# Optimization experiments

Hardware: AMD Instinct MI355X
Metric: run time of the kernel (lower is better)

## Reference

```python
import jax, jax.numpy as jnp
import numpy as np

BN_EPS = 1e-3          # nn.BatchNorm1d(..., eps=0.001)
NUM_PILLARS = 600000   # M = total occupied pillars across the batch
N_POINTS = 3_000_000
C_IN, C_OUT = 10, 64


def setup_inputs() -> dict:
    key = jax.random.key(0)
    k1, k2, k3 = jax.random.split(key, 3)
    pts_feature = jax.random.normal(k1, (N_POINTS, C_IN), dtype=jnp.float32)
    point_pillar_indices = jax.random.randint(k2, (N_POINTS,), 0, NUM_PILLARS, dtype=jnp.int32)
    # Linear(C_IN, C_OUT, bias=False), kaiming_normal init
    W = jax.random.normal(k3, (C_IN, C_OUT), dtype=jnp.float32) * np.sqrt(2.0 / C_IN)
    # BatchNorm1d in eval mode (running stats)
    gamma = jnp.ones((C_OUT,), jnp.float32)
    beta = jnp.zeros((C_OUT,), jnp.float32)
    run_mean = jnp.zeros((C_OUT,), jnp.float32)
    run_var = jnp.ones((C_OUT,), jnp.float32)
    return {"pts_feature": pts_feature, "point_pillar_indices": point_pillar_indices,
            "W": W, "gamma": gamma, "beta": beta, "run_mean": run_mean, "run_var": run_var}


def reference(pts_feature, point_pillar_indices, W, gamma, beta, run_mean, run_var):
    # shared MLP: Linear(no bias) -> BatchNorm1d(eval) -> ReLU, fused per-point
    h = pts_feature @ W                                        # (N, C_OUT)
    h = gamma * (h - run_mean) * jax.lax.rsqrt(run_var + BN_EPS) + beta
    h = jax.nn.relu(h)
    # scatter_max over irregular pillar ids -> (M, C_OUT)
    pooled = jax.ops.segment_max(h, point_pillar_indices, num_segments=NUM_PILLARS)
    # torch scatter_max leaves empty pillars at 0; jax gives -inf -> replace
    return jnp.where(jnp.isfinite(pooled), pooled, 0.0)
```

## Files before the change

kernel.cpp:

```cpp
#include <hip/hip_runtime.h>

#define C_IN 10
#define C_OUT 64
#define BN_EPS 1e-3f

#define BP    128
#define CB    256
#define NBMAX 4704
#define WIN   256
#define FSTR  12
#define MAXB  1536
#define TS    2048


__global__ __launch_bounds__(256) void k1_hist(const int* __restrict__ idx, int n, int chunk,
                                               unsigned* __restrict__ ghist, int NB) {
    __shared__ unsigned h[NBMAX];
    const int b = blockIdx.x, t = threadIdx.x;
    for (int i = t; i < NB; i += 256) h[i] = 0u;
    __syncthreads();
    const int lo = b * chunk;
    const int hi = min(n, lo + chunk);
    for (int i = lo + t; i < hi; i += 256)
        atomicAdd(&h[((unsigned)idx[i]) >> 7], 1u);
    __syncthreads();
    for (int k = t; k < NB; k += 256) ghist[(size_t)k * CB + b] = h[k];
}

__global__ __launch_bounds__(256) void k2a_reduce(const unsigned* __restrict__ g, int G,
                                                  unsigned* __restrict__ tsum) {
    __shared__ unsigned s[256];
    const int t = threadIdx.x;
    const int base = blockIdx.x * TS + t * 8;
    unsigned acc = 0;
#pragma unroll
    for (int j = 0; j < 8; ++j) { int gi = base + j; if (gi < G) acc += g[gi]; }
    s[t] = acc; __syncthreads();
    for (int off = 128; off > 0; off >>= 1) { if (t < off) s[t] += s[t + off]; __syncthreads(); }
    if (t == 0) tsum[blockIdx.x] = s[0];
}

__global__ __launch_bounds__(256) void k2b_scan(unsigned* __restrict__ tsum, int nt) {
    __shared__ unsigned partial[256], basev[256];
    const int t = threadIdx.x;
    const int per = (nt + 255) / 256;
    const int lo = t * per, hi = min(nt, lo + per);
    unsigned s = 0;
    for (int i = lo; i < hi; ++i) s += tsum[i];
    partial[t] = s; __syncthreads();
    if (t == 0) { unsigned a = 0; for (int k = 0; k < 256; ++k) { basev[k] = a; a += partial[k]; } }
    __syncthreads();
    unsigned a = basev[t];
    for (int i = lo; i < hi; ++i) { unsigned v = tsum[i]; tsum[i] = a; a += v; }
}

__global__ __launch_bounds__(256) void k2c_apply(unsigned* __restrict__ g, int G,
                                                 const unsigned* __restrict__ tsum,
                                                 unsigned* __restrict__ bstart, int NB, int n) {
    __shared__ unsigned s[256];
    const int t = threadIdx.x;
    const int base = blockIdx.x * TS + t * 8;
    unsigned v[8]; unsigned acc = 0;
#pragma unroll
    for (int j = 0; j < 8; ++j) { int gi = base + j; v[j] = (gi < G) ? g[gi] : 0u; acc += v[j]; }
    s[t] = acc; __syncthreads();
    for (int off = 1; off < 256; off <<= 1) {
        unsigned x = (t >= off) ? s[t - off] : 0u; __syncthreads();
        s[t] += x; __syncthreads();
    }
    unsigned excl = ((t == 0) ? 0u : s[t - 1]) + tsum[blockIdx.x];
#pragma unroll
    for (int j = 0; j < 8; ++j) {
        int gi = base + j;
        if (gi < G) {
            g[gi] = excl;
            if ((gi & (CB - 1)) == 0) bstart[gi / CB] = excl;
            excl += v[j];
        }
    }
    if (blockIdx.x == 0 && t == 0) bstart[NB] = (unsigned)n;
}

__global__ __launch_bounds__(256) void k3_scatter(const int* __restrict__ idx, int n, int chunk,
                                                  const unsigned* __restrict__ scanned,
                                                  unsigned* __restrict__ rec, int NB) {
    __shared__ unsigned cnt[NBMAX];
    __shared__ unsigned basel[NBMAX];
    const int b = blockIdx.x, t = threadIdx.x;
    for (int k = t; k < NB; k += 256) { basel[k] = scanned[(size_t)k * CB + b]; cnt[k] = 0u; }
    __syncthreads();
    const int lo = b * chunk, hi = min(n, lo + chunk);
    for (int i = lo + t; i < hi; i += 256) {
        unsigned pid = (unsigned)idx[i];
        unsigned k = pid >> 7;
        unsigned r = atomicAdd(&cnt[k], 1u);
        rec[basel[k] + r] = ((pid & 127u) << 22) | (unsigned)i;
    }
}

__global__ __launch_bounds__(256) void pool_sorted_kernel(
    const float* __restrict__ pts,
    const unsigned* __restrict__ rec,
    const unsigned* __restrict__ bstart,
    const float* __restrict__ W,
    const float* __restrict__ gamma, const float* __restrict__ beta,
    const float* __restrict__ mean, const float* __restrict__ var,
    float* __restrict__ out, int M)
{
    __shared__ float4  feat4[WIN * FSTR / 4];
    __shared__ unsigned seg_end[BP];
    __shared__ unsigned cnt[BP];
    __shared__ unsigned short ord[MAXB];
    __shared__ unsigned char  lpa[MAXB];
    float* feat = (float*)feat4;

    const int b = blockIdx.x;
    const int t = threadIdx.x;
    const int lane = t & 63;
    const int w = t >> 6;

    const unsigned base = bstart[b];
    const int T  = (int)(bstart[b + 1] - base);
    const int Tc = T < MAXB ? T : MAXB;
    const int npl = min(BP, M - b * BP);

    float wv[C_IN];
#pragma unroll
    for (int j = 0; j < C_IN; ++j) wv[j] = W[j * C_OUT + lane];
    const float scale = gamma[lane] * rsqrtf(var[lane] + BN_EPS);
    const float shift = fmaf(-mean[lane], scale, beta[lane]);

    if (t < BP) cnt[t] = 0u;
    __syncthreads();
    for (int r = t; r < Tc; r += 256) {
        unsigned l = rec[base + r] >> 22;
        lpa[r] = (unsigned char)l;
        atomicAdd(&cnt[l], 1u);
    }
    __syncthreads();
    if (t < BP) seg_end[t] = cnt[t];
    __syncthreads();
    for (int off = 1; off < BP; off <<= 1) {
        unsigned x = 0;
        if (t < BP && t >= off) x = seg_end[t - off];
        __syncthreads();
        if (t < BP) seg_end[t] += x;
        __syncthreads();
    }
    if (t < BP) cnt[t] = (t == 0) ? 0u : seg_end[t - 1];
    __syncthreads();
    for (int r = t; r < Tc; r += 256) {
        unsigned l = lpa[r];
        unsigned pos = atomicAdd(&cnt[l], 1u);
        ord[pos] = (unsigned short)r;
    }
    __syncthreads();

    float4 s0, s1; float2 s2; bool have = false;
    {
        const int Wn = Tc < WIN ? Tc : WIN;
        if (t < Wn) {
            unsigned rc = rec[base + ord[t]];
            const float2* f2 = (const float2*)(pts + (size_t)(rc & 0x3FFFFFu) * C_IN);
            float2 a0 = f2[0], a1 = f2[1], a2 = f2[2], a3 = f2[3], a4 = f2[4];
            s0 = make_float4(a0.x, a0.y, a1.x, a1.y);
            s1 = make_float4(a2.x, a2.y, a3.x, a3.y);
            s2 = a4; have = true;
        }
    }
    int p = w;
    float m = 0.f;
    const int nwin = (Tc + WIN - 1) / WIN;
    for (int k = 0; k < nwin; ++k) {
        const int W0 = k * WIN;
        const int Wn = (Tc - W0) < WIN ? (Tc - W0) : WIN;
        const int W1 = W0 + Wn;
        __syncthreads();
        if (have) {
            float4* fp = (float4*)&feat[t * FSTR];
            fp[0] = s0; fp[1] = s1;
            *(float2*)&feat[t * FSTR + 8] = s2;
        }
        __syncthreads();
        have = false;
        if (k + 1 < nwin) {
            const int NW0 = W0 + WIN;
            const int NWn = (Tc - NW0) < WIN ? (Tc - NW0) : WIN;
            if (t < NWn) {
                unsigned rc = rec[base + ord[NW0 + t]];
                const float2* f2 = (const float2*)(pts + (size_t)(rc & 0x3FFFFFu) * C_IN);
                float2 a0 = f2[0], a1 = f2[1], a2 = f2[2], a3 = f2[3], a4 = f2[4];
                s0 = make_float4(a0.x, a0.y, a1.x, a1.y);
                s1 = make_float4(a2.x, a2.y, a3.x, a3.y);
                s2 = a4; have = true;
            }
        }
        while (p < npl) {
            int s = (p == 0) ? 0 : (int)seg_end[p - 1];
            if (s < W0) s = W0;
            const int e = (int)seg_end[p];
            const int eh = e < W1 ? e : W1;
            int j = s;
            for (; j + 1 < eh; j += 2) {
                const float4* F0 = (const float4*)&feat[(j - W0) * FSTR];
                const float4* F1 = (const float4*)&feat[(j + 1 - W0) * FSTR];
                float4 x0 = F0[0], x1 = F0[1];
                float2 x2 = *(const float2*)&feat[(j - W0) * FSTR + 8];
                float4 y0 = F1[0], y1 = F1[1];
                float2 y2 = *(const float2*)&feat[(j + 1 - W0) * FSTR + 8];
                float h0 = 0.f, h1 = 0.f;
                h0 = fmaf(x0.x, wv[0], h0); h0 = fmaf(x0.y, wv[1], h0);
                h0 = fmaf(x0.z, wv[2], h0); h0 = fmaf(x0.w, wv[3], h0);
                h0 = fmaf(x1.x, wv[4], h0); h0 = fmaf(x1.y, wv[5], h0);
                h0 = fmaf(x1.z, wv[6], h0); h0 = fmaf(x1.w, wv[7], h0);
                h0 = fmaf(x2.x, wv[8], h0); h0 = fmaf(x2.y, wv[9], h0);
                h1 = fmaf(y0.x, wv[0], h1); h1 = fmaf(y0.y, wv[1], h1);
                h1 = fmaf(y0.z, wv[2], h1); h1 = fmaf(y0.w, wv[3], h1);
                h1 = fmaf(y1.x, wv[4], h1); h1 = fmaf(y1.y, wv[5], h1);
                h1 = fmaf(y1.z, wv[6], h1); h1 = fmaf(y1.w, wv[7], h1);
                h1 = fmaf(y2.x, wv[8], h1); h1 = fmaf(y2.y, wv[9], h1);
                h0 = fmaxf(fmaf(h0, scale, shift), 0.f);
                h1 = fmaxf(fmaf(h1, scale, shift), 0.f);
                m = fmaxf(m, fmaxf(h0, h1));
            }
            if (j < eh) {
                const float4* F0 = (const float4*)&feat[(j - W0) * FSTR];
                float4 x0 = F0[0], x1 = F0[1];
                float2 x2 = *(const float2*)&feat[(j - W0) * FSTR + 8];
                float h0 = 0.f;
                h0 = fmaf(x0.x, wv[0], h0); h0 = fmaf(x0.y, wv[1], h0);
                h0 = fmaf(x0.z, wv[2], h0); h0 = fmaf(x0.w, wv[3], h0);
                h0 = fmaf(x1.x, wv[4], h0); h0 = fmaf(x1.y, wv[5], h0);
                h0 = fmaf(x1.z, wv[6], h0); h0 = fmaf(x1.w, wv[7], h0);
                h0 = fmaf(x2.x, wv[8], h0); h0 = fmaf(x2.y, wv[9], h0);
                m = fmaxf(m, fmaxf(fmaf(h0, scale, shift), 0.f));
            }
            if (e > W1) break;
            out[((size_t)(b * BP + p)) * C_OUT + lane] = m;
            m = 0.f; p += 4;
        }
    }
    while (p < npl) {
        out[((size_t)(b * BP + p)) * C_OUT + lane] = m;
        m = 0.f; p += 4;
    }
    for (int r = MAXB; r < T; ++r) {
        unsigned rc = rec[base + r];
        const int l = (int)(rc >> 22);
        if ((l & 3) != w) continue;
        const float2* f2 = (const float2*)(pts + (size_t)(rc & 0x3FFFFFu) * C_IN);
        float2 a0 = f2[0], a1 = f2[1], a2 = f2[2], a3 = f2[3], a4 = f2[4];
        float h = 0.f;
        h = fmaf(a0.x, wv[0], h); h = fmaf(a0.y, wv[1], h);
        h = fmaf(a1.x, wv[2], h); h = fmaf(a1.y, wv[3], h);
        h = fmaf(a2.x, wv[4], h); h = fmaf(a2.y, wv[5], h);
        h = fmaf(a3.x, wv[6], h); h = fmaf(a3.y, wv[7], h);
        h = fmaf(a4.x, wv[8], h); h = fmaf(a4.y, wv[9], h);
        h = fmaxf(fmaf(h, scale, shift), 0.f);
        size_t o = ((size_t)(b * BP + l)) * C_OUT + lane;
        out[o] = fmaxf(out[o], h);
    }
}

#define CHUNK 256
#define FSTRIDE 11

__global__ __launch_bounds__(256) void zero_u32_kernel(unsigned* __restrict__ p, int n) {
    int i = blockIdx.x * 256 + threadIdx.x;
    int s = gridDim.x * 256;
    for (; i < n; i += s) p[i] = 0u;
}

__global__ __launch_bounds__(256) void hist_kernel(const int* __restrict__ idx, int n,
                                                   unsigned* __restrict__ hist, int nb) {
    __shared__ unsigned h[NBMAX];
    for (int i = threadIdx.x; i < nb; i += 256) h[i] = 0u;
    __syncthreads();
    int stride = gridDim.x * 256;
    for (int i = blockIdx.x * 256 + threadIdx.x; i < n; i += stride)
        atomicAdd(&h[((unsigned)idx[i]) >> 7], 1u);
    __syncthreads();
    for (int i = threadIdx.x; i < nb; i += 256) {
        unsigned v = h[i];
        if (v) atomicAdd(&hist[i], v);
    }
}

__global__ __launch_bounds__(256) void scan_kernel(const unsigned* __restrict__ hist,
                                                   unsigned* __restrict__ cursor, int nb) {
    __shared__ unsigned partial[256];
    __shared__ unsigned base[256];
    int per = (nb + 255) / 256;
    int lo = threadIdx.x * per;
    int hi = lo + per; if (hi > nb) hi = nb;
    unsigned s = 0;
    for (int i = lo; i < hi; ++i) s += hist[i];
    partial[threadIdx.x] = s;
    __syncthreads();
    if (threadIdx.x == 0) {
        unsigned acc = 0;
        for (int t = 0; t < 256; ++t) { base[t] = acc; acc += partial[t]; }
    }
    __syncthreads();
    unsigned acc = base[threadIdx.x];
    for (int i = lo; i < hi; ++i) { cursor[i] = acc; acc += hist[i]; }
}

__global__ __launch_bounds__(256) void scatter_ids_kernel(const int* __restrict__ idx, int n,
                                                          unsigned* __restrict__ cursor,
                                                          unsigned* __restrict__ rec) {
    int stride = gridDim.x * 256;
    for (int i = blockIdx.x * 256 + threadIdx.x; i < n; i += stride) {
        unsigned pid = (unsigned)idx[i];
        unsigned pos = atomicAdd(&cursor[pid >> 7], 1u);
        rec[pos] = ((pid & (BP - 1)) << 22) | (unsigned)i;
    }
}

__global__ __launch_bounds__(256) void pool_kernel(
    const float* __restrict__ pts, const unsigned* __restrict__ rec,
    const unsigned* __restrict__ cursor, const float* __restrict__ W,
    const float* __restrict__ gamma, const float* __restrict__ beta,
    const float* __restrict__ mean, const float* __restrict__ var,
    float* __restrict__ out, int M)
{
    __shared__ unsigned smax[BP * C_OUT];
    __shared__ float    feat[CHUNK * FSTRIDE];
    __shared__ unsigned slp[CHUNK];
    const int b = blockIdx.x, t = threadIdx.x;
    const int lane = t & 63, wid = t >> 6;
    for (int i = t; i < BP * C_OUT; i += 256) smax[i] = 0u;
    float w[C_IN];
#pragma unroll
    for (int j = 0; j < C_IN; ++j) w[j] = W[j * C_OUT + lane];
    const float scale = gamma[lane] * rsqrtf(var[lane] + BN_EPS);
    const float shift = fmaf(-mean[lane], scale, beta[lane]);
    const unsigned start = (b == 0) ? 0u : cursor[b - 1];
    const int total = (int)(cursor[b] - start);
    float fr[C_IN]; unsigned rcr = 0; bool hav = false;
    if (t < total) {
        rcr = rec[start + t];
        const float2* f2 = (const float2*)(pts + (size_t)(rcr & 0x3FFFFFu) * C_IN);
#pragma unroll
        for (int j = 0; j < 5; ++j) { float2 v = f2[j]; fr[2*j] = v.x; fr[2*j+1] = v.y; }
        hav = true;
    }
    for (int chunk = 0; chunk < total; chunk += CHUNK) {
        const int nrec = min(CHUNK, total - chunk);
        __syncthreads();
        if (hav) {
            slp[t] = rcr >> 22;
#pragma unroll
            for (int j = 0; j < C_IN; ++j) feat[t * FSTRIDE + j] = fr[j];
        }
        __syncthreads();
        const int nr = chunk + CHUNK + t;
        hav = false;
        if (nr < total) {
            rcr = rec[start + nr];
            const float2* f2 = (const float2*)(pts + (size_t)(rcr & 0x3FFFFFu) * C_IN);
#pragma unroll
            for (int j = 0; j < 5; ++j) { float2 v = f2[j]; fr[2*j] = v.x; fr[2*j+1] = v.y; }
            hav = true;
        }
        for (int i = wid; i < nrec; i += 4) {
            const unsigned lp = slp[i];
            const float* f = &feat[i * FSTRIDE];
            float h = 0.f;
#pragma unroll
            for (int j = 0; j < C_IN; ++j) h = fmaf(f[j], w[j], h);
            h = fmaxf(fmaf(h, scale, shift), 0.f);
            atomicMax(&smax[(lp << 6) + lane], __float_as_uint(h));
        }
    }
    __syncthreads();
    const float4* s4 = (const float4*)smax;
    float4* o4 = (float4*)out;
    const size_t base4 = (size_t)b * (BP * C_OUT / 4);
    const size_t tot4  = (size_t)M * (C_OUT / 4);
    for (int i = t; i < BP * C_OUT / 4; i += 256) {
        size_t g = base4 + (size_t)i;
        if (g < tot4) o4[g] = s4[i];
    }
}

__global__ __launch_bounds__(256) void zero_out_kernel(float4* __restrict__ out4, int n4) {
    int i = blockIdx.x * blockDim.x + threadIdx.x;
    int stride = gridDim.x * blockDim.x;
    float4 z = make_float4(0.f, 0.f, 0.f, 0.f);
    for (int j = i; j < n4; j += stride) out4[j] = z;
}

__global__ __launch_bounds__(256) void pillar_scatter_kernel(
    const float* __restrict__ pts, const int* __restrict__ idx,
    const float* __restrict__ W, const float* __restrict__ gamma,
    const float* __restrict__ beta, const float* __restrict__ mean,
    const float* __restrict__ var, unsigned int* __restrict__ out, int npoints)
{
    const int lane = threadIdx.x & 63;
    float w[C_IN];
#pragma unroll
    for (int j = 0; j < C_IN; ++j) w[j] = W[j * C_OUT + lane];
    const float scale = gamma[lane] * rsqrtf(var[lane] + BN_EPS);
    const float shift = fmaf(-mean[lane], scale, beta[lane]);
    const int wave_id = (blockIdx.x * blockDim.x + threadIdx.x) >> 6;
    const int nwaves  = (gridDim.x * blockDim.x) >> 6;
    for (int p = wave_id; p < npoints; p += nwaves) {
        const float* f = pts + (size_t)p * C_IN;
        float h = 0.f;
#pragma unroll
        for (int j = 0; j < C_IN; ++j) h = fmaf(f[j], w[j], h);
        h = fmaxf(fmaf(h, scale, shift), 0.f);
        atomicMax(&out[(size_t)idx[p] * C_OUT + lane], __float_as_uint(h));
    }
}


extern "C" void kernel_launch(void* const* d_in, const int* in_sizes, int n_in,
                              void* d_out, int out_size, void* d_ws, size_t ws_size,
                              hipStream_t stream) {
    const float* pts   = (const float*)d_in[0];
    const int*   idx   = (const int*)  d_in[1];
    const float* W     = (const float*)d_in[2];
    const float* gamma = (const float*)d_in[3];
    const float* beta  = (const float*)d_in[4];
    const float* mean  = (const float*)d_in[5];
    const float* var   = (const float*)d_in[6];

    const int npoints = in_sizes[0] / C_IN;
    const int M       = out_size / C_OUT;
    const int NB      = (M + BP - 1) / BP;
    const int G       = NB * CB;
    const int nt      = (G + TS - 1) / TS;
    const int chunk   = (npoints + CB - 1) / CB;

    const size_t rec_off = (((size_t)G + (size_t)nt + (size_t)NB + 1) + 63) & ~(size_t)63;
    const size_t need    = (rec_off + (size_t)npoints) * sizeof(unsigned);

    if (NB <= NBMAX && npoints < (1 << 22) && nt <= 65535 && ws_size >= need) {
        unsigned* ghist  = (unsigned*)d_ws;
        unsigned* tsum   = ghist + G;
        unsigned* bstart = tsum + nt;
        unsigned* rec    = (unsigned*)d_ws + rec_off;

        k1_hist          <<<CB, 256, 0, stream>>>(idx, npoints, chunk, ghist, NB);
        k2a_reduce       <<<nt, 256, 0, stream>>>(ghist, G, tsum);
        k2b_scan         <<<1,  256, 0, stream>>>(tsum, nt);
        k2c_apply        <<<nt, 256, 0, stream>>>(ghist, G, tsum, bstart, NB, npoints);
        k3_scatter       <<<CB, 256, 0, stream>>>(idx, npoints, chunk, ghist, rec, NB);
        pool_sorted_kernel<<<NB, 256, 0, stream>>>(pts, rec, bstart, W, gamma, beta,
                                                   mean, var, (float*)d_out, M);
        return;
    }

    const size_t rec_off_f1 = ((size_t)(2 * NB) + 63) & ~(size_t)63;
    const size_t need_f1    = (rec_off_f1 + (size_t)npoints) * sizeof(unsigned);
    if (NB <= NBMAX && npoints < (1 << 22) && ws_size >= need_f1) {
        unsigned* cursor = (unsigned*)d_ws;
        unsigned* hist   = cursor + NB;
        unsigned* rec    = (unsigned*)d_ws + rec_off_f1;
        zero_u32_kernel<<<(2 * NB + 255) / 256, 256, 0, stream>>>(cursor, 2 * NB);
        hist_kernel<<<256, 256, 0, stream>>>(idx, npoints, hist, NB);
        scan_kernel<<<1, 256, 0, stream>>>(hist, cursor, NB);
        scatter_ids_kernel<<<2048, 256, 0, stream>>>(idx, npoints, cursor, rec);
        pool_kernel<<<NB, 256, 0, stream>>>(pts, rec, cursor, W, gamma, beta, mean, var,
                                            (float*)d_out, M);
        return;
    }

    zero_out_kernel<<<2048, 256, 0, stream>>>((float4*)d_out, out_size / 4);
    pillar_scatter_kernel<<<2048, 256, 0, stream>>>(
        pts, idx, W, gamma, beta, mean, var, (unsigned int*)d_out, npoints);
}
```

Baseline: 243.9 us.

## Replace per-pillar FMA pooling with bf16 MFMA and shared-memory atomicMax pooling

Rewrites the pooling kernel to stage each 256-point window as bf16 A-fragments and compute the 10->64 linear plus folded BatchNorm (scale in weights, shift via a constant-1 column) with 16x16x32 bf16 MFMA instructions. The max is then taken with LDS atomicMax on the float bits into a per-block 128x64 table, which is valid because ReLU makes every value non-negative. This removes the in-block counting sort, prefix scan and MAXB overflow path, and the table is written out with vectorized stores. The trade is that inputs and weights are rounded to bf16, which loses precision against the fp32 reference, and there are now many LDS atomic operations per point.

```diff
diff --git a/kernel.cpp b/kernel.cpp
--- a/kernel.cpp
+++ b/kernel.cpp
@@ -1,4 +1,5 @@
 #include <hip/hip_runtime.h>
+#include <hip/hip_bf16.h>
 
 #define C_IN 10
 #define C_OUT 64
@@ -7,10 +8,10 @@
 #define BP    128
 #define CB    256
 #define NBMAX 4704
-#define WIN   256
-#define FSTR  12
-#define MAXB  1536
 #define TS    2048
+
+typedef __attribute__((ext_vector_type(8))) short bf16x8;
+typedef __attribute__((ext_vector_type(4))) float f32x4;
 
 
 __global__ __launch_bounds__(256) void k1_hist(const int* __restrict__ idx, int n, int chunk,
@@ -98,7 +99,13 @@
     }
 }
 
-__global__ __launch_bounds__(256) void pool_sorted_kernel(
+
+static __device__ __forceinline__ unsigned pk2(float2 v) {
+    __hip_bfloat162 h = __float22bfloat162_rn(v);
+    return *reinterpret_cast<unsigned*>(&h);
+}
+
+__global__ __launch_bounds__(256) void pool_mfma_kernel(
     const float* __restrict__ pts,
     const unsigned* __restrict__ rec,
     const unsigned* __restrict__ bstart,
@@ -107,158 +114,115 @@
     const float* __restrict__ mean, const float* __restrict__ var,
     float* __restrict__ out, int M)
 {
-    __shared__ float4  feat4[WIN * FSTR / 4];
-    __shared__ unsigned seg_end[BP];
-    __shared__ unsigned cnt[BP];
-    __shared__ unsigned short ord[MAXB];
-    __shared__ unsigned char  lpa[MAXB];
-    float* feat = (float*)feat4;
+    __shared__ unsigned smax[129 * 64];
+    __shared__ unsigned astage[256 * 20];
+    __shared__ unsigned char slp[256];
 
     const int b = blockIdx.x;
     const int t = threadIdx.x;
     const int lane = t & 63;
     const int w = t >> 6;
+    const int g  = lane >> 4;
+    const int c0 = lane & 15;
+
+    {
+        uint4* s4 = (uint4*)smax;
+        const uint4 z = make_uint4(0, 0, 0, 0);
+        for (int i = t; i < 129 * 16; i += 256) s4[i] = z;
+    }
+
+    bf16x8 bfrag[4];
+#pragma unroll
+    for (int tc = 0; tc < 4; ++tc) {
+        const int ch = 16 * tc + c0;
+        const float sc = gamma[ch] * rsqrtf(var[ch] + BN_EPS);
+        const float sh = fmaf(-mean[ch], sc, beta[ch]);
+        union { bf16x8 v; unsigned short u[8]; } B;
+#pragma unroll
+        for (int j = 0; j < 8; ++j) {
+            const int k = g * 8 + j;
+            float val = 0.f;
+            if (k < 10) val = W[k * C_OUT + ch] * sc;
+            else if (k == 10) val = sh;
+            __hip_bfloat16 hb = __float2bfloat16(val);
+            B.u[j] = *reinterpret_cast<unsigned short*>(&hb);
+        }
+        bfrag[tc] = B.v;
+    }
 
     const unsigned base = bstart[b];
-    const int T  = (int)(bstart[b + 1] - base);
-    const int Tc = T < MAXB ? T : MAXB;
-    const int npl = min(BP, M - b * BP);
-
-    float wv[C_IN];
-#pragma unroll
-    for (int j = 0; j < C_IN; ++j) wv[j] = W[j * C_OUT + lane];
-    const float scale = gamma[lane] * rsqrtf(var[lane] + BN_EPS);
-    const float shift = fmaf(-mean[lane], scale, beta[lane]);
-
-    if (t < BP) cnt[t] = 0u;
-    __syncthreads();
-    for (int r = t; r < Tc; r += 256) {
-        unsigned l = rec[base + r] >> 22;
-        lpa[r] = (unsigned char)l;
-        atomicAdd(&cnt[l], 1u);
-    }
-    __syncthreads();
-    if (t < BP) seg_end[t] = cnt[t];
-    __syncthreads();
-    for (int off = 1; off < BP; off <<= 1) {
-        unsigned x = 0;
-        if (t < BP && t >= off) x = seg_end[t - off];
+    const int T = (int)(bstart[b + 1] - base);
+    const int nwin = (T + 255) >> 8;
+
+    float2 pf0, pf1, pf2, pf3, pf4;
+    unsigned prec = 0; bool have = false;
+    if (t < T) {
+        prec = rec[base + t];
+        const float2* f2 = (const float2*)(pts + (size_t)(prec & 0x3FFFFFu) * C_IN);
+        pf0 = f2[0]; pf1 = f2[1]; pf2 = f2[2]; pf3 = f2[3]; pf4 = f2[4];
+        have = true;
+    }
+
+    for (int k = 0; k < nwin; ++k) {
         __syncthreads();
-        if (t < BP) seg_end[t] += x;
-        __syncthreads();
-    }
-    if (t < BP) cnt[t] = (t == 0) ? 0u : seg_end[t - 1];
-    __syncthreads();
-    for (int r = t; r < Tc; r += 256) {
-        unsigned l = lpa[r];
-        unsigned pos = atomicAdd(&cnt[l], 1u);
-        ord[pos] = (unsigned short)r;
-    }
-    __syncthreads();
-
-    float4 s0, s1; float2 s2; bool have = false;
-    {
-        const int Wn = Tc < WIN ? Tc : WIN;
-        if (t < Wn) {
-            unsigned rc = rec[base + ord[t]];
-            const float2* f2 = (const float2*)(pts + (size_t)(rc & 0x3FFFFFu) * C_IN);
-            float2 a0 = f2[0], a1 = f2[1], a2 = f2[2], a3 = f2[3], a4 = f2[4];
-            s0 = make_float4(a0.x, a0.y, a1.x, a1.y);
-            s1 = make_float4(a2.x, a2.y, a3.x, a3.y);
-            s2 = a4; have = true;
-        }
-    }
-    int p = w;
-    float m = 0.f;
-    const int nwin = (Tc + WIN - 1) / WIN;
-    for (int k = 0; k < nwin; ++k) {
-        const int W0 = k * WIN;
-        const int Wn = (Tc - W0) < WIN ? (Tc - W0) : WIN;
-        const int W1 = W0 + Wn;
-        __syncthreads();
-        if (have) {
-            float4* fp = (float4*)&feat[t * FSTR];
-            fp[0] = s0; fp[1] = s1;
-            *(float2*)&feat[t * FSTR + 8] = s2;
+        {
+            uint4* ap = (uint4*)&astage[(unsigned)t * 20];
+            const uint4 z = make_uint4(0, 0, 0, 0);
+            if (have) {
+                slp[t] = (unsigned char)(prec >> 22);
+                ap[0] = make_uint4(pk2(pf0), pk2(pf1), pk2(pf2), pk2(pf3));
+                ap[1] = make_uint4(pk2(pf4), 0x00003F80u , 0u, 0u);
+            } else {
+                slp[t] = 128;
+                ap[0] = z; ap[1] = z;
+            }
+            ap[2] = z; ap[3] = z;
         }
         __syncthreads();
         have = false;
-        if (k + 1 < nwin) {
-            const int NW0 = W0 + WIN;
-            const int NWn = (Tc - NW0) < WIN ? (Tc - NW0) : WIN;
-            if (t < NWn) {
-                unsigned rc = rec[base + ord[NW0 + t]];
-                const float2* f2 = (const float2*)(pts + (size_t)(rc & 0x3FFFFFu) * C_IN);
-                float2 a0 = f2[0], a1 = f2[1], a2 = f2[2], a3 = f2[3], a4 = f2[4];
-                s0 = make_float4(a0.x, a0.y, a1.x, a1.y);
-                s1 = make_float4(a2.x, a2.y, a3.x, a3.y);
-                s2 = a4; have = true;
+        {
+            const int nr = (k + 1) * 256 + t;
+            if (nr < T) {
+                prec = rec[base + nr];
+                const float2* f2 = (const float2*)(pts + (size_t)(prec & 0x3FFFFFu) * C_IN);
+                pf0 = f2[0]; pf1 = f2[1]; pf2 = f2[2]; pf3 = f2[3]; pf4 = f2[4];
+                have = true;
             }
         }
-        while (p < npl) {
-            int s = (p == 0) ? 0 : (int)seg_end[p - 1];
-            if (s < W0) s = W0;
-            const int e = (int)seg_end[p];
-            const int eh = e < W1 ? e : W1;
-            int j = s;
-            for (; j + 1 < eh; j += 2) {
-                const float4* F0 = (const float4*)&feat[(j - W0) * FSTR];
-                const float4* F1 = (const float4*)&feat[(j + 1 - W0) * FSTR];
-                float4 x0 = F0[0], x1 = F0[1];
-                float2 x2 = *(const float2*)&feat[(j - W0) * FSTR + 8];
-                float4 y0 = F1[0], y1 = F1[1];
-                float2 y2 = *(const float2*)&feat[(j + 1 - W0) * FSTR + 8];
-                float h0 = 0.f, h1 = 0.f;
-                h0 = fmaf(x0.x, wv[0], h0); h0 = fmaf(x0.y, wv[1], h0);
-                h0 = fmaf(x0.z, wv[2], h0); h0 = fmaf(x0.w, wv[3], h0);
-                h0 = fmaf(x1.x, wv[4], h0); h0 = fmaf(x1.y, wv[5], h0);
-                h0 = fmaf(x1.z, wv[6], h0); h0 = fmaf(x1.w, wv[7], h0);
-                h0 = fmaf(x2.x, wv[8], h0); h0 = fmaf(x2.y, wv[9], h0);
-                h1 = fmaf(y0.x, wv[0], h1); h1 = fmaf(y0.y, wv[1], h1);
-                h1 = fmaf(y0.z, wv[2], h1); h1 = fmaf(y0.w, wv[3], h1);
-                h1 = fmaf(y1.x, wv[4], h1); h1 = fmaf(y1.y, wv[5], h1);
-                h1 = fmaf(y1.z, wv[6], h1); h1 = fmaf(y1.w, wv[7], h1);
-                h1 = fmaf(y2.x, wv[8], h1); h1 = fmaf(y2.y, wv[9], h1);
-                h0 = fmaxf(fmaf(h0, scale, shift), 0.f);
-                h1 = fmaxf(fmaf(h1, scale, shift), 0.f);
-                m = fmaxf(m, fmaxf(h0, h1));
+#pragma unroll
+        for (int ti = 0; ti < 4; ++ti) {
+            const int tbase = (4 * w + ti) * 16;
+            union { uint4 q; bf16x8 v; } A;
+            A.q = *(const uint4*)&astage[(unsigned)(tbase + c0) * 20 + (unsigned)(g * 4)];
+            const f32x4 z4 = {0.f, 0.f, 0.f, 0.f};
+            f32x4 a0 = __builtin_amdgcn_mfma_f32_16x16x32_bf16(A.v, bfrag[0], z4, 0, 0, 0);
+            f32x4 a1 = __builtin_amdgcn_mfma_f32_16x16x32_bf16(A.v, bfrag[1], z4, 0, 0, 0);
+            f32x4 a2 = __builtin_amdgcn_mfma_f32_16x16x32_bf16(A.v, bfrag[2], z4, 0, 0, 0);
+            f32x4 a3 = __builtin_amdgcn_mfma_f32_16x16x32_bf16(A.v, bfrag[3], z4, 0, 0, 0);
+#pragma unroll
+            for (int r = 0; r < 4; ++r) {
+                const int pt = tbase + g * 4 + r;
+                const unsigned lp = slp[pt];
+                unsigned* srow = &smax[lp * 64 + c0];
+                atomicMax(&srow[0],  __float_as_uint(fmaxf(a0[r], 0.f)));
+                atomicMax(&srow[16], __float_as_uint(fmaxf(a1[r], 0.f)));
+                atomicMax(&srow[32], __float_as_uint(fmaxf(a2[r], 0.f)));
+                atomicMax(&srow[48], __float_as_uint(fmaxf(a3[r], 0.f)));
             }
-            if (j < eh) {
-                const float4* F0 = (const float4*)&feat[(j - W0) * FSTR];
-                float4 x0 = F0[0], x1 = F0[1];
-                float2 x2 = *(const float2*)&feat[(j - W0) * FSTR + 8];
-                float h0 = 0.f;
-                h0 = fmaf(x0.x, wv[0], h0); h0 = fmaf(x0.y, wv[1], h0);
-                h0 = fmaf(x0.z, wv[2], h0); h0 = fmaf(x0.w, wv[3], h0);
-                h0 = fmaf(x1.x, wv[4], h0); h0 = fmaf(x1.y, wv[5], h0);
-                h0 = fmaf(x1.z, wv[6], h0); h0 = fmaf(x1.w, wv[7], h0);
-                h0 = fmaf(x2.x, wv[8], h0); h0 = fmaf(x2.y, wv[9], h0);
-                m = fmaxf(m, fmaxf(fmaf(h0, scale, shift), 0.f));
-            }
-            if (e > W1) break;
-            out[((size_t)(b * BP + p)) * C_OUT + lane] = m;
-            m = 0.f; p += 4;
-        }
-    }
-    while (p < npl) {
-        out[((size_t)(b * BP + p)) * C_OUT + lane] = m;
-        m = 0.f; p += 4;
-    }
-    for (int r = MAXB; r < T; ++r) {
-        unsigned rc = rec[base + r];
-        const int l = (int)(rc >> 22);
-        if ((l & 3) != w) continue;
-        const float2* f2 = (const float2*)(pts + (size_t)(rc & 0x3FFFFFu) * C_IN);
-        float2 a0 = f2[0], a1 = f2[1], a2 = f2[2], a3 = f2[3], a4 = f2[4];
-        float h = 0.f;
-        h = fmaf(a0.x, wv[0], h); h = fmaf(a0.y, wv[1], h);
-        h = fmaf(a1.x, wv[2], h); h = fmaf(a1.y, wv[3], h);
-        h = fmaf(a2.x, wv[4], h); h = fmaf(a2.y, wv[5], h);
-        h = fmaf(a3.x, wv[6], h); h = fmaf(a3.y, wv[7], h);
-        h = fmaf(a4.x, wv[8], h); h = fmaf(a4.y, wv[9], h);
-        h = fmaxf(fmaf(h, scale, shift), 0.f);
-        size_t o = ((size_t)(b * BP + l)) * C_OUT + lane;
-        out[o] = fmaxf(out[o], h);
+        }
+    }
+    __syncthreads();
+
+    const uint4* s4 = (const uint4*)smax;
+    float4* o4 = (float4*)out;
+    const size_t base4 = (size_t)b * (BP * C_OUT / 4);
+    const size_t tot4  = (size_t)M * (C_OUT / 4);
+    for (int i = t; i < BP * C_OUT / 4; i += 256) {
+        size_t gi = base4 + (size_t)i;
+        if (gi < tot4) {
+            uint4 v = s4[i];
+            o4[gi] = *reinterpret_cast<float4*>(&v);
+        }
     }
 }
 
@@ -448,8 +412,8 @@
         k2b_scan         <<<1,  256, 0, stream>>>(tsum, nt);
         k2c_apply        <<<nt, 256, 0, stream>>>(ghist, G, tsum, bstart, NB, npoints);
         k3_scatter       <<<CB, 256, 0, stream>>>(idx, npoints, chunk, ghist, rec, NB);
-        pool_sorted_kernel<<<NB, 256, 0, stream>>>(pts, rec, bstart, W, gamma, beta,
-                                                   mean, var, (float*)d_out, M);
+        pool_mfma_kernel <<<NB, 256, 0, stream>>>(pts, rec, bstart, W, gamma, beta,
+                                                  mean, var, (float*)d_out, M);
         return;
     }
 
```

Measured after the change: 219.4 us. 1.11x faster.
